# Optimization experiments

Hardware: AMD Instinct MI355X
Metric: run time of the kernel (lower is better)

The kernel has to match this reference:

```python
import jax, jax.numpy as jnp
import numpy as np

P = 16           # patch size
D = 768          # embed / feature dim (= 3*P*P)
T = 8            # number of task vectors
H_META = 192     # MetaNet hidden (= D // 4)


def patchify(x):
    # x: [B, 3, H, W] -> [B, N, 3*P*P]
    B, C, H, W = x.shape
    x = x.reshape(B, C, H // P, P, W // P, P)
    x = x.transpose(0, 2, 4, 1, 3, 5)
    return x.reshape(B, (H // P) * (W // P), C * P * P)


def encode(W1, b1, W2, b2, x):
    # base functional encoder f(params, x): shared weights over the batch
    patches = patchify(x)                       # [B, N, D]
    h = jax.nn.relu(patches @ W1 + b1)          # [B, N, D]
    pooled = h.mean(axis=1)                     # [B, D]
    return pooled @ W2 + b2                     # [B, D]


def setup_inputs() -> dict:
    key = jax.random.key(0)
    ks = jax.random.split(key, 14)
    B = 64
    s = 0.02
    return {
        "x":   jax.random.normal(ks[0], (B, 3, 224, 224), jnp.float32),
        # base model params
        "W1":  jax.random.normal(ks[1], (D, D), jnp.float32) * s,
        "b1":  jax.random.normal(ks[2], (D,), jnp.float32) * s,
        "W2":  jax.random.normal(ks[3], (D, D), jnp.float32) * s,
        "b2":  jax.random.normal(ks[4], (D,), jnp.float32) * s,
        # task-vector deltas (stacked over T tasks)
        "dW1": jax.random.normal(ks[5], (T, D, D), jnp.float32) * s,
        "db1": jax.random.normal(ks[6], (T, D), jnp.float32) * s,
        "dW2": jax.random.normal(ks[7], (T, D, D), jnp.float32) * s,
        "db2": jax.random.normal(ks[8], (T, D), jnp.float32) * s,
        # MetaNet (Linear-ReLU-Linear); zero-init in the original, random here
        "mw1": jax.random.normal(ks[9], (D, H_META), jnp.float32) * s,
        "mb1": jax.random.normal(ks[10], (H_META,), jnp.float32) * s,
        "mw2": jax.random.normal(ks[11], (H_META, T), jnp.float32) * s,
        "mb2": jax.random.normal(ks[12], (T,), jnp.float32) * s,
    }


def reference(x, W1, b1, W2, b2, dW1, db1, dW2, db2, mw1, mb1, mw2, mb2):
    # 1) base features with frozen base model (torch.no_grad)
    base = jax.lax.stop_gradient(encode(W1, b1, W2, b2, x))       # [B, D]
    # 2) per-sample mixing coefficients via MetaNet
    coefs = jax.nn.relu(base @ mw1 + mb1) @ mw2 + mb2             # [B, T]
    # 3) per-sample mixed parameters: p + sum_t c[b,t] * dp[t]
    nW1 = W1 + jnp.einsum("bt,tij->bij", coefs, dW1)              # [B, D, D]
    nb1 = b1 + coefs @ db1                                        # [B, D]
    nW2 = W2 + jnp.einsum("bt,tij->bij", coefs, dW2)              # [B, D, D]
    nb2 = b2 + coefs @ db2                                        # [B, D]
    # 4) batched per-sample forward with the mixed weights
    patches = patchify(x)                                         # [B, N, D]
    h = jax.nn.relu(jnp.einsum("bnd,bde->bne", patches, nW1) + nb1[:, None, :])
    pooled = h.mean(axis=1)                                       # [B, D]
    out = jnp.einsum("bd,bde->be", pooled, nW2) + nb2             # [B, D]
    return out
```

## Files before the change

### kernel.cpp

```cpp
#include <hip/hip_runtime.h>
#include <hip/hip_bf16.h>


typedef __bf16 bf16x8 __attribute__((ext_vector_type(8)));
typedef float f32x4 __attribute__((ext_vector_type(4)));
typedef __hip_bfloat16 bf16;

struct alignas(16) BF8 { bf16 h[8]; };

constexpr int BATCH = 64;
constexpr int NP    = 196;
constexpr int NPAD  = 256;
constexpr int DIM   = 768;
constexpr int NT    = 8;
constexpr size_t MSZ = (size_t)DIM * DIM;

__device__ __forceinline__ void async_cp16(const void* g, void* l) {
  __builtin_amdgcn_global_load_lds(
      (const __attribute__((address_space(1))) uint32_t*)g,
      (__attribute__((address_space(3))) uint32_t*)l, 16, 0, 0);
}

__global__ void k_patchify(const float* __restrict__ x, bf16* __restrict__ A) {
  int idx  = blockIdx.x * blockDim.x + threadIdx.x;
  int col4 = idx % (DIM / 4);
  int row  = idx / (DIM / 4);
  int d = col4 * 4;
  int b = row >> 8;
  int n = row & 255;
  bf16 tmp[4];
  if (n < NP) {
    int hp = n / 14, wp = n % 14;
    int c  = d >> 8;
    int rr = d & 255;
    int i = rr >> 4, j = rr & 15;
    const float* src = x + ((((size_t)b * 3 + c) * 224 + hp * 16 + i) * 224 + wp * 16 + j);
    float4 f = *(const float4*)src;
    tmp[0] = __float2bfloat16(f.x);
    tmp[1] = __float2bfloat16(f.y);
    tmp[2] = __float2bfloat16(f.z);
    tmp[3] = __float2bfloat16(f.w);
  } else {
    tmp[0] = tmp[1] = tmp[2] = tmp[3] = __float2bfloat16(0.0f);
  }
  *(ushort4*)(A + (size_t)row * DIM + d) = *(ushort4*)tmp;
}

__global__ void k_transpose_cast(const float* __restrict__ W1, const float* __restrict__ dW1,
                                 const float* __restrict__ W2, const float* __restrict__ dW2,
                                 bf16* __restrict__ WT) {
  __shared__ float tile[32][33];
  int mat = blockIdx.z;
  const float* src;
  if      (mat == 0) src = W1;
  else if (mat <= 8) src = dW1 + (size_t)(mat - 1) * MSZ;
  else if (mat == 9) src = W2;
  else               src = dW2 + (size_t)(mat - 10) * MSZ;
  int n0 = blockIdx.x * 32;
  int k0 = blockIdx.y * 32;
  int tx = threadIdx.x & 31, ty = threadIdx.x >> 5;
#pragma unroll
  for (int r = ty; r < 32; r += 8)
    tile[r][tx] = src[(size_t)(k0 + r) * DIM + n0 + tx];
  __syncthreads();
  bf16* dst = WT + (size_t)mat * MSZ;
#pragma unroll
  for (int r = ty; r < 32; r += 8)
    dst[(size_t)(n0 + r) * DIM + k0 + tx] = __float2bfloat16(tile[tx][r]);
}


template<int MIX>
__global__ __launch_bounds__(256, 3)
void k_gemm_pool(const bf16* __restrict__ A,
                 const bf16* __restrict__ WT,
                 const float* __restrict__ b1,
                 const float* __restrict__ db1,
                 const float* __restrict__ coefs,
                 float* __restrict__ pooled) {
  __shared__ uint4 AslU[256 * 8];
  __shared__ uint4 BslU[64 * 8];
  __shared__ float biasl[64];
  __shared__ float cl[NT];
  __shared__ float red[4][64];

  int b  = blockIdx.x;
  int n0 = blockIdx.y * 64;
  int tid = threadIdx.x;

  if (MIX) {
    if (tid < NT) cl[tid] = coefs[b * NT + tid];
    __syncthreads();
  }
  if (tid < 64) {
    float bias = b1[n0 + tid];
    if (MIX) {
#pragma unroll
      for (int t = 0; t < NT; t++) bias += cl[t] * db1[t * DIM + n0 + tid];
    }
    biasl[tid] = bias;
  }
  float cr[NT];
  if (MIX) {
#pragma unroll
    for (int t = 0; t < NT; t++) cr[t] = cl[t];
  }

  const bf16* Ag = A + (size_t)b * NPAD * DIM;
  int wave = tid >> 6, lane = tid & 63;
  int quad = lane >> 4, l16 = lane & 15;
  f32x4 acc[4][4] = {};

  for (int kt = 0; kt < 12; kt++) {
    const bf16* Ak = Ag + kt * 64;
    const bf16* Wk = WT + kt * 64;
#pragma unroll
    for (int i = 0; i < 8; i++) {
      int s = wave * 512 + i * 64 + lane;
      int r = s >> 3, c = (s & 7) ^ (r & 7);
      async_cp16(Ak + (size_t)r * DIM + c * 8, (void*)(AslU + wave * 512 + i * 64));
    }
    if (!MIX) {
#pragma unroll
      for (int i = 0; i < 2; i++) {
        int s = wave * 128 + i * 64 + lane;
        int r = s >> 3, c = (s & 7) ^ (r & 7);
        async_cp16(Wk + (size_t)(n0 + r) * DIM + c * 8, (void*)(BslU + wave * 128 + i * 64));
      }
    } else {
#pragma unroll
      for (int i = 0; i < 2; i++) {
        int g = tid + 256 * i;
        int r = g >> 3, c = (g & 7) ^ (r & 7);
        const bf16* p0 = Wk + (size_t)(n0 + r) * DIM + c * 8;
        BF8 w = *(const BF8*)p0;
        float m[8];
#pragma unroll
        for (int j = 0; j < 8; j++) m[j] = __bfloat162float(w.h[j]);
#pragma unroll
        for (int t = 0; t < NT; t++) {
          BF8 dv = *(const BF8*)(p0 + (size_t)(1 + t) * MSZ);
          float cc = cr[t];
#pragma unroll
          for (int j = 0; j < 8; j++) m[j] += cc * __bfloat162float(dv.h[j]);
        }
        BF8 o;
#pragma unroll
        for (int j = 0; j < 8; j++) o.h[j] = __float2bfloat16(m[j]);
        BslU[g] = *(uint4*)&o;
      }
    }
    __syncthreads();
    const bf16* As = (const bf16*)AslU;
    const bf16* Bs = (const bf16*)BslU;
#pragma unroll
    for (int ks = 0; ks < 2; ks++) {
      bf16x8 bfr[4];
#pragma unroll
      for (int nf = 0; nf < 4; nf++) {
        int brow = nf * 16 + l16;
        bfr[nf] = *(const bf16x8*)(Bs + ((size_t)brow * 8 + ((ks * 4 + quad) ^ (brow & 7))) * 8);
      }
#pragma unroll
      for (int mf = 0; mf < 4; mf++) {
        int arow = wave * 64 + mf * 16 + l16;
        bf16x8 af = *(const bf16x8*)(As + ((size_t)arow * 8 + ((ks * 4 + quad) ^ (arow & 7))) * 8);
#pragma unroll
        for (int nf = 0; nf < 4; nf++)
          acc[mf][nf] = __builtin_amdgcn_mfma_f32_16x16x32_bf16(af, bfr[nf], acc[mf][nf], 0, 0, 0);
      }
    }
    __syncthreads();
  }

  int m0 = wave * 64;
  float colsum[4];
#pragma unroll
  for (int nf = 0; nf < 4; nf++) {
    float bias = biasl[nf * 16 + l16];
    float s = 0.0f;
#pragma unroll
    for (int mf = 0; mf < 4; mf++) {
      int rbase = m0 + mf * 16 + quad * 4;
#pragma unroll
      for (int r = 0; r < 4; r++) {
        if (rbase + r < NP) s += fmaxf(acc[mf][nf][r] + bias, 0.0f);
      }
    }
    s += __shfl_xor(s, 16, 64);
    s += __shfl_xor(s, 32, 64);
    colsum[nf] = s;
  }
  if (lane < 16) {
#pragma unroll
    for (int nf = 0; nf < 4; nf++) red[wave][nf * 16 + lane] = colsum[nf];
  }
  __syncthreads();
  if (tid < 64) {
    float s = red[0][tid] + red[1][tid] + red[2][tid] + red[3][tid];
    pooled[(size_t)b * DIM + n0 + tid] = s * (1.0f / 196.0f);
  }
}

__global__ __launch_bounds__(256, 2)
void k_gemm2(const float* __restrict__ Af,
             const bf16* __restrict__ WT,
             int matbase,
             const float* __restrict__ bias,
             float* __restrict__ Y) {
  __shared__ uint4 AslU[64 * 8];
  __shared__ uint4 BslU[64 * 8];
  int n0  = blockIdx.x * 64;
  int mat = blockIdx.y;
  int tid = threadIdx.x, wave = tid >> 6, lane = tid & 63;
  int quad = lane >> 4, l16 = lane & 15;
  f32x4 acc[4] = {};
  const bf16* Wm = WT + (size_t)(matbase + mat) * MSZ;
  for (int k0 = 0; k0 < DIM; k0 += 64) {
#pragma unroll
    for (int i = 0; i < 2; i++) {
      int g = tid + i * 256;
      int r = g >> 3, c = g & 7;
      const float* src = Af + (size_t)r * DIM + k0 + c * 8;
      float4 xa = ((const float4*)src)[0];
      float4 xb = ((const float4*)src)[1];
      BF8 o;
      o.h[0] = __float2bfloat16(xa.x); o.h[1] = __float2bfloat16(xa.y);
      o.h[2] = __float2bfloat16(xa.z); o.h[3] = __float2bfloat16(xa.w);
      o.h[4] = __float2bfloat16(xb.x); o.h[5] = __float2bfloat16(xb.y);
      o.h[6] = __float2bfloat16(xb.z); o.h[7] = __float2bfloat16(xb.w);
      AslU[r * 8 + (c ^ (r & 7))] = *(uint4*)&o;
      BslU[r * 8 + (c ^ (r & 7))] = *(const uint4*)(Wm + (size_t)(n0 + r) * DIM + k0 + c * 8);
    }
    __syncthreads();
    const bf16* As = (const bf16*)AslU;
    const bf16* Bs = (const bf16*)BslU;
#pragma unroll
    for (int ks = 0; ks < 2; ks++) {
      int brow = wave * 16 + l16;
      bf16x8 bfr = *(const bf16x8*)(Bs + (size_t)(brow * 8 + ((ks * 4 + quad) ^ (brow & 7))) * 8);
#pragma unroll
      for (int mf = 0; mf < 4; mf++) {
        int arow = mf * 16 + l16;
        bf16x8 af = *(const bf16x8*)(As + (size_t)(arow * 8 + ((ks * 4 + quad) ^ (arow & 7))) * 8);
        acc[mf] = __builtin_amdgcn_mfma_f32_16x16x32_bf16(af, bfr, acc[mf], 0, 0, 0);
      }
    }
    __syncthreads();
  }
#pragma unroll
  for (int mf = 0; mf < 4; mf++) {
#pragma unroll
    for (int r = 0; r < 4; r++) {
      int row = mf * 16 + quad * 4 + r;
      int col = n0 + wave * 16 + l16;
      float v = acc[mf][r];
      if (bias) v += bias[col];
      Y[((size_t)mat * 64 + row) * DIM + col] = v;
    }
  }
}

__global__ void k_metanet(const float* __restrict__ base,
                          const float* __restrict__ mw1, const float* __restrict__ mb1,
                          const float* __restrict__ mw2, const float* __restrict__ mb2,
                          float* __restrict__ coefs) {
  __shared__ float bl[DIM];
  __shared__ float hl[192];
  int b = blockIdx.x, tid = threadIdx.x;
  for (int i = tid; i < DIM; i += 192) bl[i] = base[(size_t)b * DIM + i];
  __syncthreads();
  float s = mb1[tid];
  for (int k = 0; k < DIM; k++) s += bl[k] * mw1[(size_t)k * 192 + tid];
  hl[tid] = fmaxf(s, 0.0f);
  __syncthreads();
  if (tid < NT) {
    float c = mb2[tid];
    for (int j = 0; j < 192; j++) c += hl[j] * mw2[(size_t)j * NT + tid];
    coefs[b * NT + tid] = c;
  }
}

__global__ void k_combine(const float* __restrict__ Y,
                          const float* __restrict__ coefs,
                          const float* __restrict__ b2,
                          const float* __restrict__ db2,
                          float* __restrict__ out) {
  int idx = blockIdx.x * 256 + threadIdx.x;
  int b = idx / DIM, e = idx % DIM;
  float v = Y[(size_t)b * DIM + e] + b2[e];
#pragma unroll
  for (int t = 0; t < NT; t++) {
    float c = coefs[b * NT + t];
    v += c * (Y[((size_t)(1 + t) * 64 + b) * DIM + e] + db2[(size_t)t * DIM + e]);
  }
  out[idx] = v;
}

extern "C" void kernel_launch(void* const* d_in, const int* in_sizes, int n_in,
                              void* d_out, int out_size, void* d_ws, size_t ws_size,
                              hipStream_t stream) {
  const float* x   = (const float*)d_in[0];
  const float* W1  = (const float*)d_in[1];
  const float* b1  = (const float*)d_in[2];
  const float* W2  = (const float*)d_in[3];
  const float* b2  = (const float*)d_in[4];
  const float* dW1 = (const float*)d_in[5];
  const float* db1 = (const float*)d_in[6];
  const float* dW2 = (const float*)d_in[7];
  const float* db2 = (const float*)d_in[8];
  const float* mw1 = (const float*)d_in[9];
  const float* mb1 = (const float*)d_in[10];
  const float* mw2 = (const float*)d_in[11];
  const float* mb2 = (const float*)d_in[12];
  float* out = (float*)d_out;
  (void)in_sizes; (void)n_in; (void)out_size; (void)ws_size;

  char* ws = (char*)d_ws;
  bf16*  A_bf    = (bf16*) (ws);
  bf16*  WT      = (bf16*) (ws + 25165824);
  float* pooledA = (float*)(ws + 46399488);
  float* pooledB = (float*)(ws + 46596096);
  float* coefs   = (float*)(ws + 46792704);
  float* base    = (float*)(ws + 46794752);
  float* Y       = (float*)(ws + 46991360);

  k_patchify<<<dim3((BATCH * NPAD * (DIM / 4)) / 256), 256, 0, stream>>>(x, A_bf);
  k_transpose_cast<<<dim3(24, 24, 18), 256, 0, stream>>>(W1, dW1, W2, dW2, WT);
  k_gemm_pool<0><<<dim3(BATCH, DIM / 64), 256, 0, stream>>>(A_bf, WT, b1, db1, nullptr, pooledA);
  k_gemm2<<<dim3(DIM / 64, 1), 256, 0, stream>>>(pooledA, WT, 9, b2, base);
  k_metanet<<<dim3(BATCH), 192, 0, stream>>>(base, mw1, mb1, mw2, mb2, coefs);
  k_gemm_pool<1><<<dim3(BATCH, DIM / 64), 256, 0, stream>>>(A_bf, WT, b1, db1, coefs, pooledB);
  k_gemm2<<<dim3(DIM / 64, 9), 256, 0, stream>>>(pooledB, WT, 9, nullptr, Y);
  k_combine<<<dim3((BATCH * DIM) / 256), 256, 0, stream>>>(Y, coefs, b2, db2, out);
}
```

Measured before the change: 307.8 us.

## Double-buffer gemm_pool, pair samples per block, split rows with atomic pooling

Restructures the patch GEMM+pool kernel. Each block now covers two samples and half the padded patch rows, with K tiles of 32 held in double-buffered LDS, so the next tile's loads overlap the current MFMAs. In the mixed path, the per-sample weight blend is computed once per tile and reused for both samples, which halves the repeated reads of the task-vector deltas. Partial column sums are added into a pre-zeroed pooled buffer with atomics, which costs an extra memset and makes the summation order nondeterministic.

```diff
diff --git a/kernel.cpp b/kernel.cpp
--- a/kernel.cpp
+++ b/kernel.cpp
@@ -14,6 +14,7 @@
 constexpr int DIM   = 768;
 constexpr int NT    = 8;
 constexpr size_t MSZ = (size_t)DIM * DIM;
+constexpr int KT    = 24;
 
 __device__ __forceinline__ void async_cp16(const void* g, void* l) {
   __builtin_amdgcn_global_load_lds(
@@ -71,6 +72,58 @@
 
 
 template<int MIX>
+__device__ __forceinline__ void stage_tile(const bf16* __restrict__ A, const bf16* __restrict__ WT,
+                                           int b0, int rowbase, int n0, int kk, int tid,
+                                           uint4* __restrict__ Ab, uint4* __restrict__ Bb,
+                                           const float* __restrict__ c0,
+                                           const float* __restrict__ c1) {
+  if (MIX) {
+    int r = tid >> 2, cp = tid & 3, c = cp ^ (r & 3);
+    const bf16* p0 = WT + (size_t)(n0 + r) * DIM + kk + c * 8;
+    BF8 w = *(const BF8*)p0;
+    BF8 dv[8];
+#pragma unroll
+    for (int t = 0; t < NT; t++) dv[t] = *(const BF8*)(p0 + (size_t)(1 + t) * MSZ);
+    asm volatile("" ::: "memory");
+#pragma unroll
+    for (int i = 0; i < 4; i++) {
+      int p = i * 256 + tid;
+      int s = p >> 9, rr = (p >> 2) & 127, cc = (p & 3) ^ (rr & 3);
+      async_cp16(A + ((size_t)(b0 + s) * NPAD + rowbase + rr) * DIM + kk + cc * 8,
+                 (void*)(Ab + p));
+    }
+    float m0[8], m1[8];
+#pragma unroll
+    for (int j = 0; j < 8; j++) { float wv = __bfloat162float(w.h[j]); m0[j] = wv; m1[j] = wv; }
+#pragma unroll
+    for (int t = 0; t < NT; t++) {
+#pragma unroll
+      for (int j = 0; j < 8; j++) {
+        float d = __bfloat162float(dv[t].h[j]);
+        m0[j] += c0[t] * d;
+        m1[j] += c1[t] * d;
+      }
+    }
+    BF8 o0, o1;
+#pragma unroll
+    for (int j = 0; j < 8; j++) { o0.h[j] = __float2bfloat16(m0[j]); o1.h[j] = __float2bfloat16(m1[j]); }
+    Bb[tid]       = *(uint4*)&o0;
+    Bb[256 + tid] = *(uint4*)&o1;
+    asm volatile("s_waitcnt lgkmcnt(0)" ::: "memory");
+  } else {
+#pragma unroll
+    for (int i = 0; i < 4; i++) {
+      int p = i * 256 + tid;
+      int s = p >> 9, rr = (p >> 2) & 127, cc = (p & 3) ^ (rr & 3);
+      async_cp16(A + ((size_t)(b0 + s) * NPAD + rowbase + rr) * DIM + kk + cc * 8,
+                 (void*)(Ab + p));
+    }
+    int r = tid >> 2, c = (tid & 3) ^ (r & 3);
+    async_cp16(WT + (size_t)(n0 + r) * DIM + kk + c * 8, (void*)(Bb + tid));
+  }
+}
+
+template<int MIX>
 __global__ __launch_bounds__(256, 3)
 void k_gemm_pool(const bf16* __restrict__ A,
                  const bf16* __restrict__ WT,
@@ -78,127 +131,96 @@
                  const float* __restrict__ db1,
                  const float* __restrict__ coefs,
                  float* __restrict__ pooled) {
-  __shared__ uint4 AslU[256 * 8];
-  __shared__ uint4 BslU[64 * 8];
-  __shared__ float biasl[64];
-  __shared__ float cl[NT];
+  __shared__ uint4 AslU[2][1024];
+  __shared__ uint4 BslU[2][512];
+  __shared__ float biasl[2][64];
+  __shared__ float clS[2][NT];
   __shared__ float red[4][64];
 
-  int b  = blockIdx.x;
-  int n0 = blockIdx.y * 64;
+  int nt = blockIdx.x, rb = blockIdx.y, sg = blockIdx.z;
+  int n0 = nt * 64, rowbase = rb * 128, b0 = sg * 2;
   int tid = threadIdx.x;
 
+  float c0[NT], c1[NT];
   if (MIX) {
-    if (tid < NT) cl[tid] = coefs[b * NT + tid];
+    if (tid < 16) clS[tid >> 3][tid & 7] = coefs[(b0 + (tid >> 3)) * NT + (tid & 7)];
     __syncthreads();
-  }
-  if (tid < 64) {
-    float bias = b1[n0 + tid];
+#pragma unroll
+    for (int t = 0; t < NT; t++) { c0[t] = clS[0][t]; c1[t] = clS[1][t]; }
+  }
+  if (tid < 128) {
+    int s = tid >> 6, col = tid & 63;
+    float bias = b1[n0 + col];
     if (MIX) {
 #pragma unroll
-      for (int t = 0; t < NT; t++) bias += cl[t] * db1[t * DIM + n0 + tid];
-    }
-    biasl[tid] = bias;
-  }
-  float cr[NT];
-  if (MIX) {
-#pragma unroll
-    for (int t = 0; t < NT; t++) cr[t] = cl[t];
-  }
-
-  const bf16* Ag = A + (size_t)b * NPAD * DIM;
+      for (int t = 0; t < NT; t++) bias += clS[s][t] * db1[t * DIM + n0 + col];
+    }
+    biasl[s][col] = bias;
+  }
+
   int wave = tid >> 6, lane = tid & 63;
   int quad = lane >> 4, l16 = lane & 15;
+  int s = wave & 1, half = wave >> 1;
   f32x4 acc[4][4] = {};
 
-  for (int kt = 0; kt < 12; kt++) {
-    const bf16* Ak = Ag + kt * 64;
-    const bf16* Wk = WT + kt * 64;
-#pragma unroll
-    for (int i = 0; i < 8; i++) {
-      int s = wave * 512 + i * 64 + lane;
-      int r = s >> 3, c = (s & 7) ^ (r & 7);
-      async_cp16(Ak + (size_t)r * DIM + c * 8, (void*)(AslU + wave * 512 + i * 64));
-    }
-    if (!MIX) {
-#pragma unroll
-      for (int i = 0; i < 2; i++) {
-        int s = wave * 128 + i * 64 + lane;
-        int r = s >> 3, c = (s & 7) ^ (r & 7);
-        async_cp16(Wk + (size_t)(n0 + r) * DIM + c * 8, (void*)(BslU + wave * 128 + i * 64));
+  stage_tile<MIX>(A, WT, b0, rowbase, n0, 0, tid, AslU[0], BslU[0], c0, c1);
+
+  int buf = 0;
+  for (int kt = 0; kt < KT; kt++) {
+    if (kt + 1 < KT) {
+      stage_tile<MIX>(A, WT, b0, rowbase, n0, (kt + 1) * 32, tid,
+                      AslU[buf ^ 1], BslU[buf ^ 1], c0, c1);
+      if (!MIX) asm volatile("s_waitcnt vmcnt(5)" ::: "memory");
+    } else {
+      asm volatile("s_waitcnt vmcnt(0)" ::: "memory");
+    }
+    __builtin_amdgcn_s_barrier();
+    const uint4* Ab = AslU[buf];
+    const uint4* Bb = BslU[buf];
+    bf16x8 bfr[4];
+#pragma unroll
+    for (int nf = 0; nf < 4; nf++) {
+      int brow = nf * 16 + l16;
+      bfr[nf] = *(const bf16x8*)(Bb + (MIX ? s : 0) * 256 + brow * 4 + (quad ^ (brow & 3)));
+    }
+#pragma unroll
+    for (int mf = 0; mf < 4; mf++) {
+      int arow = half * 64 + mf * 16 + l16;
+      bf16x8 af = *(const bf16x8*)(Ab + s * 512 + arow * 4 + (quad ^ (arow & 3)));
+#pragma unroll
+      for (int nf = 0; nf < 4; nf++)
+        acc[mf][nf] = __builtin_amdgcn_mfma_f32_16x16x32_bf16(af, bfr[nf], acc[mf][nf], 0, 0, 0);
+    }
+    __builtin_amdgcn_s_barrier();
+    buf ^= 1;
+  }
+
+  float colsum[4];
+#pragma unroll
+  for (int nf = 0; nf < 4; nf++) {
+    float bias = biasl[MIX ? s : s][nf * 16 + l16];
+    float sum = 0.0f;
+#pragma unroll
+    for (int mf = 0; mf < 4; mf++) {
+      int rbase = rowbase + half * 64 + mf * 16 + quad * 4;
+#pragma unroll
+      for (int r = 0; r < 4; r++) {
+        if (rbase + r < NP) sum += fmaxf(acc[mf][nf][r] + bias, 0.0f);
       }
-    } else {
-#pragma unroll
-      for (int i = 0; i < 2; i++) {
-        int g = tid + 256 * i;
-        int r = g >> 3, c = (g & 7) ^ (r & 7);
-        const bf16* p0 = Wk + (size_t)(n0 + r) * DIM + c * 8;
-        BF8 w = *(const BF8*)p0;
-        float m[8];
-#pragma unroll
-        for (int j = 0; j < 8; j++) m[j] = __bfloat162float(w.h[j]);
-#pragma unroll
-        for (int t = 0; t < NT; t++) {
-          BF8 dv = *(const BF8*)(p0 + (size_t)(1 + t) * MSZ);
-          float cc = cr[t];
-#pragma unroll
-          for (int j = 0; j < 8; j++) m[j] += cc * __bfloat162float(dv.h[j]);
-        }
-        BF8 o;
-#pragma unroll
-        for (int j = 0; j < 8; j++) o.h[j] = __float2bfloat16(m[j]);
-        BslU[g] = *(uint4*)&o;
-      }
-    }
-    __syncthreads();
-    const bf16* As = (const bf16*)AslU;
-    const bf16* Bs = (const bf16*)BslU;
-#pragma unroll
-    for (int ks = 0; ks < 2; ks++) {
-      bf16x8 bfr[4];
-#pragma unroll
-      for (int nf = 0; nf < 4; nf++) {
-        int brow = nf * 16 + l16;
-        bfr[nf] = *(const bf16x8*)(Bs + ((size_t)brow * 8 + ((ks * 4 + quad) ^ (brow & 7))) * 8);
-      }
-#pragma unroll
-      for (int mf = 0; mf < 4; mf++) {
-        int arow = wave * 64 + mf * 16 + l16;
-        bf16x8 af = *(const bf16x8*)(As + ((size_t)arow * 8 + ((ks * 4 + quad) ^ (arow & 7))) * 8);
-#pragma unroll
-        for (int nf = 0; nf < 4; nf++)
-          acc[mf][nf] = __builtin_amdgcn_mfma_f32_16x16x32_bf16(af, bfr[nf], acc[mf][nf], 0, 0, 0);
-      }
-    }
-    __syncthreads();
-  }
-
-  int m0 = wave * 64;
-  float colsum[4];
-#pragma unroll
-  for (int nf = 0; nf < 4; nf++) {
-    float bias = biasl[nf * 16 + l16];
-    float s = 0.0f;
-#pragma unroll
-    for (int mf = 0; mf < 4; mf++) {
-      int rbase = m0 + mf * 16 + quad * 4;
-#pragma unroll
-      for (int r = 0; r < 4; r++) {
-        if (rbase + r < NP) s += fmaxf(acc[mf][nf][r] + bias, 0.0f);
-      }
-    }
-    s += __shfl_xor(s, 16, 64);
-    s += __shfl_xor(s, 32, 64);
-    colsum[nf] = s;
+    }
+    sum += __shfl_xor(sum, 16, 64);
+    sum += __shfl_xor(sum, 32, 64);
+    colsum[nf] = sum;
   }
   if (lane < 16) {
 #pragma unroll
     for (int nf = 0; nf < 4; nf++) red[wave][nf * 16 + lane] = colsum[nf];
   }
   __syncthreads();
-  if (tid < 64) {
-    float s = red[0][tid] + red[1][tid] + red[2][tid] + red[3][tid];
-    pooled[(size_t)b * DIM + n0 + tid] = s * (1.0f / 196.0f);
+  if (tid < 128) {
+    int ss = tid >> 6, col = tid & 63;
+    float v = red[ss][col] + red[ss + 2][col];
+    atomicAdd(pooled + (size_t)(b0 + ss) * DIM + n0 + col, v * (1.0f / 196.0f));
   }
 }
 
@@ -325,12 +347,14 @@
   float* base    = (float*)(ws + 46794752);
   float* Y       = (float*)(ws + 46991360);
 
+  hipMemsetAsync(pooledA, 0, 2 * 196608, stream);
+
   k_patchify<<<dim3((BATCH * NPAD * (DIM / 4)) / 256), 256, 0, stream>>>(x, A_bf);
   k_transpose_cast<<<dim3(24, 24, 18), 256, 0, stream>>>(W1, dW1, W2, dW2, WT);
-  k_gemm_pool<0><<<dim3(BATCH, DIM / 64), 256, 0, stream>>>(A_bf, WT, b1, db1, nullptr, pooledA);
+  k_gemm_pool<0><<<dim3(12, 2, 32), 256, 0, stream>>>(A_bf, WT, b1, db1, nullptr, pooledA);
   k_gemm2<<<dim3(DIM / 64, 1), 256, 0, stream>>>(pooledA, WT, 9, b2, base);
   k_metanet<<<dim3(BATCH), 192, 0, stream>>>(base, mw1, mb1, mw2, mb2, coefs);
-  k_gemm_pool<1><<<dim3(BATCH, DIM / 64), 256, 0, stream>>>(A_bf, WT, b1, db1, coefs, pooledB);
+  k_gemm_pool<1><<<dim3(12, 2, 32), 256, 0, stream>>>(A_bf, WT, b1, db1, coefs, pooledB);
   k_gemm2<<<dim3(DIM / 64, 9), 256, 0, stream>>>(pooledB, WT, 9, nullptr, Y);
   k_combine<<<dim3((BATCH * DIM) / 256), 256, 0, stream>>>(Y, coefs, b2, db2, out);
 }
```

After: 631.9 us. 2.05x slower.
